# Kernel tuning notes

Hardware: AMD Instinct MI355X
Metric: run time of the kernel (lower is better)

## Reference

```python
import jax, jax.numpy as jnp
import numpy as np

D_MODEL = 1024
N_HEADS = 16
D_HEAD = D_MODEL // N_HEADS
B, T = 4, 2048


def setup_inputs() -> dict:
    key = jax.random.key(0)
    k1, k2, k3 = jax.random.split(key, 3)
    x = jax.random.normal(k1, (B, T, D_MODEL), dtype=jnp.float32)
    # nn.Linear(d_model, 3*d_model, bias=False): y = x @ W_qkv (stored here as [d, 3d])
    W_qkv = jax.random.normal(k2, (D_MODEL, 3 * D_MODEL), dtype=jnp.float32) * (D_MODEL ** -0.5)
    W_out = jax.random.normal(k3, (D_MODEL, D_MODEL), dtype=jnp.float32) * (D_MODEL ** -0.5)
    # causal mask: 1 = keep, 0 = masked (masked_fill(mask == 0, -inf))
    mask = jnp.tril(jnp.ones((T, T), dtype=jnp.int32))
    return {"x": x, "W_qkv": W_qkv, "W_out": W_out, "mask": mask}


def reference(x, W_qkv, W_out, mask):
    Bb, Tt, C = x.shape
    qkv = (x @ W_qkv).reshape(Bb, Tt, 3, N_HEADS, D_HEAD)
    q, k, v = qkv[:, :, 0], qkv[:, :, 1], qkv[:, :, 2]  # each [B,T,H,Dh]
    # scores: [B,H,T,T]
    attn = jnp.einsum('bthd,bshd->bhts', q, k) / jnp.sqrt(jnp.float32(D_HEAD))
    attn = jnp.where(mask == 0, -jnp.inf, attn)
    attn = jax.nn.softmax(attn, axis=-1)
    out = jnp.einsum('bhts,bshd->bthd', attn, v).reshape(Bb, Tt, C)
    return out @ W_out
```

## Files before the change

kernel.cpp:

```cpp
#include <hip/hip_runtime.h>
#include <cstdint>
#include <cstddef>


#define D_MODEL 1024
#define NHEADS  16
#define DHEAD   64
#define BATCH   4
#define SEQ     2048

typedef __attribute__((ext_vector_type(8))) _Float16 half8;
typedef __attribute__((ext_vector_type(4))) _Float16 half4;
typedef __attribute__((ext_vector_type(4))) float    f32x4;

__device__ __forceinline__ void async_copy16(const _Float16* g, _Float16* l) {
    __builtin_amdgcn_global_load_lds(
        (const __attribute__((address_space(1))) uint32_t*)g,
        (__attribute__((address_space(3))) uint32_t*)l, 16, 0, 0);
}

__device__ __forceinline__ float fast_exp2(float x) {
#if __has_builtin(__builtin_amdgcn_exp2f)
    return __builtin_amdgcn_exp2f(x);
#else
    return exp2f(x);
#endif
}

__global__ void cast_f32_f16(const float* __restrict__ in,
                             _Float16* __restrict__ out) {
    int i = blockIdx.x * blockDim.x + threadIdx.x;
    float4 v = *(const float4*)(in + (size_t)i * 4);
    half4 o;
    o.x = (_Float16)v.x; o.y = (_Float16)v.y;
    o.z = (_Float16)v.z; o.w = (_Float16)v.w;
    *(half4*)(out + (size_t)i * 4) = o;
}

__global__ void transpose_cast(const float* __restrict__ in,
                               _Float16* __restrict__ out, int R, int C) {
    __shared__ float tile[32][33];
    int c0 = blockIdx.x * 32, r0 = blockIdx.y * 32;
    int tx = threadIdx.x, ty = threadIdx.y;
    #pragma unroll
    for (int i = 0; i < 32; i += 8)
        tile[ty + i][tx] = in[(size_t)(r0 + ty + i) * C + c0 + tx];
    __syncthreads();
    #pragma unroll
    for (int i = 0; i < 32; i += 8)
        out[(size_t)(c0 + ty + i) * R + r0 + tx] = (_Float16)tile[tx][ty + i];
}

__global__ void gemm_qkv(const _Float16* __restrict__ A,
                         const _Float16* __restrict__ Bt,
                         _Float16* __restrict__ QK,
                         _Float16* __restrict__ Vtg) {
    __shared__ __attribute__((aligned(16))) _Float16 smem[128 * 132];
    _Float16* As = smem;
    _Float16* Bs = smem + 8192;

    const int tid  = threadIdx.x;
    const int w    = tid >> 6, lane = tid & 63;
    const int l15  = lane & 15, quad = lane >> 4;
    const int wm   = w >> 1, wn = w & 1;
    const int row0 = blockIdx.y * 128, col0 = blockIdx.x * 128;
    const int K = 1024;

    f32x4 acc[4][4];
    #pragma unroll
    for (int i = 0; i < 4; i++)
        #pragma unroll
        for (int j = 0; j < 4; j++)
            acc[i][j] = (f32x4){0.f, 0.f, 0.f, 0.f};

    const int lr  = lane >> 3;
    const int src = (lane & 7) ^ lr;

    for (int k0 = 0; k0 < K; k0 += 64) {
        __syncthreads();
        #pragma unroll
        for (int q = 0; q < 4; q++) {
            async_copy16(A  + (size_t)(row0 + q * 32 + w * 8 + lr) * K + k0 + src * 8,
                         &As[(q * 32 + w * 8) * 64]);
            async_copy16(Bt + (size_t)(col0 + q * 32 + w * 8 + lr) * K + k0 + src * 8,
                         &Bs[(q * 32 + w * 8) * 64]);
        }
        __syncthreads();

        half8 af[2][4], bfm[2][4];
        #pragma unroll
        for (int i = 0; i < 4; i++) {
            const int ar = wm * 64 + i * 16 + l15;
            const int rs = ar & 7;
            #pragma unroll
            for (int kk = 0; kk < 2; kk++)
                af[kk][i] = *(const half8*)&As[ar * 64 + ((kk * 4 + quad) ^ rs) * 8];
        }
        #pragma unroll
        for (int j = 0; j < 4; j++) {
            const int br = wn * 64 + j * 16 + l15;
            const int rs = br & 7;
            #pragma unroll
            for (int kk = 0; kk < 2; kk++)
                bfm[kk][j] = *(const half8*)&Bs[br * 64 + ((kk * 4 + quad) ^ rs) * 8];
        }
        #pragma unroll
        for (int kk = 0; kk < 2; kk++)
            #pragma unroll
            for (int i = 0; i < 4; i++)
                #pragma unroll
                for (int j = 0; j < 4; j++)
                    acc[i][j] = __builtin_amdgcn_mfma_f32_16x16x32_f16(
                        af[kk][i], bfm[kk][j], acc[i][j], 0, 0, 0);
    }

    if (blockIdx.x < 16) {
        #pragma unroll
        for (int i = 0; i < 4; i++) {
            int row = row0 + wm * 64 + i * 16 + quad * 4;
            #pragma unroll
            for (int j = 0; j < 4; j++) {
                int col = col0 + wn * 64 + j * 16 + l15;
                #pragma unroll
                for (int r = 0; r < 4; r++)
                    QK[(size_t)(row + r) * 2048 + col] = (_Float16)acc[i][j][r];
            }
        }
    } else {
        __syncthreads();
        #pragma unroll
        for (int i = 0; i < 4; i++) {
            int tl = wm * 64 + i * 16 + quad * 4;
            #pragma unroll
            for (int j = 0; j < 4; j++) {
                int vl = wn * 64 + j * 16 + l15;
                half4 pk;
                #pragma unroll
                for (int r = 0; r < 4; r++) pk[r] = (_Float16)acc[i][j][r];
                *(half4*)&smem[vl * 132 + tl] = pk;
            }
        }
        __syncthreads();
        const int bb = row0 >> 11, tb = row0 & 2047;
        const int rr0 = tid >> 4;
        const int cc  = (tid & 15) * 8;
        #pragma unroll
        for (int s = 0; s < 8; s++) {
            int vl = rr0 + s * 16;
            int vcol = (col0 - 2048) + vl;
            int hh = vcol >> 6, d = vcol & 63;
            *(half8*)&Vtg[((size_t)((bb * 16 + hh) * 64 + d)) * 2048 + tb + cc] =
                *(const half8*)&smem[vl * 132 + cc];
        }
    }
}

__global__ void gemm_out(const _Float16* __restrict__ A,
                         const _Float16* __restrict__ Bt,
                         float* __restrict__ Cf, int N, int K) {
    __shared__ __attribute__((aligned(16))) _Float16 As[128 * 32];
    __shared__ __attribute__((aligned(16))) _Float16 Bs[128 * 32];

    const int tid  = threadIdx.x;
    const int w    = tid >> 6, lane = tid & 63;
    const int l15  = lane & 15, quad = lane >> 4;
    const int wm   = w >> 1, wn = w & 1;
    const int row0 = blockIdx.y * 128, col0 = blockIdx.x * 128;

    f32x4 acc[4][4];
    #pragma unroll
    for (int i = 0; i < 4; i++)
        #pragma unroll
        for (int j = 0; j < 4; j++)
            acc[i][j] = (f32x4){0.f, 0.f, 0.f, 0.f};

    const int r0i = tid >> 2, c0i = tid & 3;
    const int r1i = (256 + tid) >> 2;

    for (int k0 = 0; k0 < K; k0 += 32) {
        __syncthreads();
        async_copy16(A  + (size_t)(row0 + r0i) * K + k0 + c0i * 8, &As[(w * 64) * 8]);
        async_copy16(A  + (size_t)(row0 + r1i) * K + k0 + c0i * 8, &As[(256 + w * 64) * 8]);
        async_copy16(Bt + (size_t)(col0 + r0i) * K + k0 + c0i * 8, &Bs[(w * 64) * 8]);
        async_copy16(Bt + (size_t)(col0 + r1i) * K + k0 + c0i * 8, &Bs[(256 + w * 64) * 8]);
        __syncthreads();

        half8 af[4], bfm[4];
        #pragma unroll
        for (int i = 0; i < 4; i++)
            af[i] = *(const half8*)&As[(wm * 64 + i * 16 + l15) * 32 + quad * 8];
        #pragma unroll
        for (int j = 0; j < 4; j++)
            bfm[j] = *(const half8*)&Bs[(wn * 64 + j * 16 + l15) * 32 + quad * 8];
        #pragma unroll
        for (int i = 0; i < 4; i++)
            #pragma unroll
            for (int j = 0; j < 4; j++)
                acc[i][j] = __builtin_amdgcn_mfma_f32_16x16x32_f16(
                    af[i], bfm[j], acc[i][j], 0, 0, 0);
    }

    #pragma unroll
    for (int i = 0; i < 4; i++) {
        int row = row0 + wm * 64 + i * 16 + quad * 4;
        #pragma unroll
        for (int j = 0; j < 4; j++) {
            int col = col0 + wn * 64 + j * 16 + l15;
            #pragma unroll
            for (int r = 0; r < 4; r++)
                Cf[(size_t)(row + r) * N + col] = acc[i][j][r];
        }
    }
}

#define PREFETCH(t)                                                          \
    do {                                                                     \
        const _Float16* kp_ = kb + (size_t)((t) * 128 + srow) * 2048 + sc;   \
        kr0 = *(const half8*)kp_;                                            \
        kr1 = *(const half8*)(kp_ + (size_t)32 * 2048);                      \
        kr2 = *(const half8*)(kp_ + (size_t)64 * 2048);                      \
        kr3 = *(const half8*)(kp_ + (size_t)96 * 2048);                      \
        const _Float16* vp_ = vb + (size_t)srow * 2048 + (t) * 128 + sc;     \
        vr0 = *(const half8*)vp_;                                            \
        vr1 = *(const half8*)(vp_ + 64);                                     \
        vr2 = *(const half8*)(vp_ + (size_t)32 * 2048);                      \
        vr3 = *(const half8*)(vp_ + (size_t)32 * 2048 + 64);                 \
    } while (0)

__global__ __launch_bounds__(256, 2) void flash_attn(
        const _Float16* __restrict__ qk, const _Float16* __restrict__ vt,
        _Float16* __restrict__ obuf) {
    const int h = blockIdx.x, pr = blockIdx.y, b = blockIdx.z;
    const int tid = threadIdx.x;
    const int w = tid >> 6, lane = tid & 63;
    const int l15 = lane & 15, quad = lane >> 4;

    __shared__ __attribute__((aligned(16))) _Float16 Ks[128 * 72];
    __shared__ __attribute__((aligned(16))) _Float16 Vs[64 * 136];
    __shared__ __attribute__((aligned(16))) _Float16 Pl[4][32 * 136];

    const _Float16* kb = qk + (size_t)b * SEQ * 2048 + D_MODEL + h * 64;
    const _Float16* vb = vt + (size_t)(b * 16 + h) * 64 * 2048;

    const int srow = tid >> 3;
    const int sc   = (tid & 7) * 8;

    const _Float16 QSCL = (_Float16)0.18033688f;

    #pragma unroll 1
    for (int phase = 0; phase < 2; ++phase) {
        const int tq = phase ? (15 - pr) : pr;
        const int q0 = tq * 128;
        const int n_iter = tq + 1;

        half8 qf[2][2];
        #pragma unroll
        for (int g = 0; g < 2; g++) {
            const _Float16* qp = qk
                + ((size_t)(b * SEQ + q0 + w * 32 + g * 16 + l15)) * 2048
                + h * DHEAD + quad * 8;
            qf[g][0] = *(const half8*)qp;
            qf[g][1] = *(const half8*)(qp + 32);
            #pragma unroll
            for (int j = 0; j < 8; j++) {
                qf[g][0][j] *= QSCL;
                qf[g][1][j] *= QSCL;
            }
        }

        f32x4 o[2][4];
        float l_acc[2] = {0.f, 0.f};
        #pragma unroll
        for (int g = 0; g < 2; g++)
            #pragma unroll
            for (int d = 0; d < 4; d++) o[g][d] = (f32x4){0.f, 0.f, 0.f, 0.f};

        half8 kr0, kr1, kr2, kr3, vr0, vr1, vr2, vr3;
        PREFETCH(0);

        #pragma unroll 1
        for (int it = 0; it < n_iter; ++it) {
            __syncthreads();
            *(half8*)&Ks[(srow      ) * 72 + sc] = kr0;
            *(half8*)&Ks[(srow + 32 ) * 72 + sc] = kr1;
            *(half8*)&Ks[(srow + 64 ) * 72 + sc] = kr2;
            *(half8*)&Ks[(srow + 96 ) * 72 + sc] = kr3;
            *(half8*)&Vs[srow * 136 + sc]             = vr0;
            *(half8*)&Vs[srow * 136 + sc + 64]        = vr1;
            *(half8*)&Vs[(srow + 32) * 136 + sc]      = vr2;
            *(half8*)&Vs[(srow + 32) * 136 + sc + 64] = vr3;
            __syncthreads();

            if (it + 1 < n_iter) PREFETCH(it + 1);

            #pragma unroll
            for (int hh = 0; hh < 2; hh++) {
                f32x4 st[2][4];
                __builtin_amdgcn_s_setprio(1);
                #pragma unroll
                for (int n4 = 0; n4 < 4; n4++) {
                    const int nt = hh * 4 + n4;
                    half8 ka0 = *(const half8*)&Ks[(nt * 16 + l15) * 72 + quad * 8];
                    half8 ka1 = *(const half8*)&Ks[(nt * 16 + l15) * 72 + 32 + quad * 8];
                    #pragma unroll
                    for (int g = 0; g < 2; g++) {
                        f32x4 acc = (f32x4){0.f, 0.f, 0.f, 0.f};
                        acc = __builtin_amdgcn_mfma_f32_16x16x32_f16(ka0, qf[g][0], acc, 0, 0, 0);
                        acc = __builtin_amdgcn_mfma_f32_16x16x32_f16(ka1, qf[g][1], acc, 0, 0, 0);
                        st[g][n4] = acc;
                    }
                }
                __builtin_amdgcn_s_setprio(0);

                #pragma unroll
                for (int g = 0; g < 2; g++) {
                    const int c0 = __builtin_amdgcn_readfirstlane(
                        q0 + w * 32 + g * 16 - 128 * it);
                    if (c0 < 127) {
                        #pragma unroll
                        for (int n4 = 0; n4 < 4; n4++)
                            #pragma unroll
                            for (int r = 0; r < 4; r++)
                                if ((hh * 4 + n4) * 16 + quad * 4 + r - l15 > c0)
                                    st[g][n4][r] = -INFINITY;
                    }
                    #pragma unroll
                    for (int n4 = 0; n4 < 4; n4++) {
                        const int nt = hh * 4 + n4;
                        float p0 = fast_exp2(st[g][n4][0]);
                        float p1 = fast_exp2(st[g][n4][1]);
                        float p2 = fast_exp2(st[g][n4][2]);
                        float p3 = fast_exp2(st[g][n4][3]);
                        l_acc[g] += (p0 + p1) + (p2 + p3);
                        auto lo = __builtin_amdgcn_cvt_pkrtz(p0, p1);
                        auto hi = __builtin_amdgcn_cvt_pkrtz(p2, p3);
                        half4 pk;
                        pk[0] = (_Float16)lo[0]; pk[1] = (_Float16)lo[1];
                        pk[2] = (_Float16)hi[0]; pk[3] = (_Float16)hi[1];
                        *(half4*)&Pl[w][(g * 16 + l15) * 136 + nt * 16 + quad * 4] = pk;
                    }
                }
            }
            asm volatile("s_waitcnt lgkmcnt(0)" ::: "memory");

            __builtin_amdgcn_s_setprio(1);
            #pragma unroll
            for (int kf = 0; kf < 4; kf++) {
                half8 pf0 = *(const half8*)&Pl[w][l15 * 136 + kf * 32 + quad * 8];
                half8 pf1 = *(const half8*)&Pl[w][(16 + l15) * 136 + kf * 32 + quad * 8];
                #pragma unroll
                for (int dt = 0; dt < 4; dt++) {
                    half8 vf = *(const half8*)&Vs[(dt * 16 + l15) * 136 + kf * 32 + quad * 8];
                    o[0][dt] = __builtin_amdgcn_mfma_f32_16x16x32_f16(pf0, vf, o[0][dt], 0, 0, 0);
                    o[1][dt] = __builtin_amdgcn_mfma_f32_16x16x32_f16(pf1, vf, o[1][dt], 0, 0, 0);
                }
            }
            __builtin_amdgcn_s_setprio(0);
        }

        #pragma unroll
        for (int g = 0; g < 2; g++) {
            float l = l_acc[g];
            l += __shfl_xor(l, 16);
            l += __shfl_xor(l, 32);
            float linv[4];
            #pragma unroll
            for (int r = 0; r < 4; r++)
                linv[r] = 1.0f / __shfl(l, quad * 4 + r, 16);

            _Float16* ob = obuf
                + ((size_t)(b * SEQ + q0 + w * 32 + g * 16 + quad * 4)) * D_MODEL
                + h * DHEAD;
            #pragma unroll
            for (int r = 0; r < 4; r++) {
                #pragma unroll
                for (int dt = 0; dt < 4; dt++)
                    ob[(size_t)r * D_MODEL + dt * 16 + l15] =
                        (_Float16)(o[g][dt][r] * linv[r]);
            }
        }
        __syncthreads();
    }
}

extern "C" void kernel_launch(void* const* d_in, const int* in_sizes, int n_in,
                              void* d_out, int out_size, void* d_ws, size_t ws_size,
                              hipStream_t stream) {
    const float* x    = (const float*)d_in[0];
    const float* Wqkv = (const float*)d_in[1];
    const float* Wout = (const float*)d_in[2];
    float* out = (float*)d_out;

    char* ws = (char*)d_ws;
    _Float16* Xh   = (_Float16*)(ws);
    _Float16* WqT  = (_Float16*)(ws + ((size_t)16 << 20));
    _Float16* WoT  = (_Float16*)(ws + ((size_t)23 << 20));
    _Float16* QKb  = (_Float16*)(ws + ((size_t)26 << 20));
    _Float16* Vtg  = (_Float16*)(ws + ((size_t)58 << 20));
    _Float16* Obuf = (_Float16*)(ws + ((size_t)74 << 20));

    cast_f32_f16<<<8192, 256, 0, stream>>>(x, Xh);
    transpose_cast<<<dim3(96, 32), dim3(32, 8), 0, stream>>>(Wqkv, WqT, 1024, 3072);
    transpose_cast<<<dim3(32, 32), dim3(32, 8), 0, stream>>>(Wout, WoT, 1024, 1024);
    gemm_qkv<<<dim3(24, 64), 256, 0, stream>>>(Xh, WqT, QKb, Vtg);
    flash_attn<<<dim3(NHEADS, 8, BATCH), 256, 0, stream>>>(QKb, Vtg, Obuf);
    gemm_out<<<dim3(8, 64), 256, 0, stream>>>(Obuf, WoT, out, 1024, 1024);
}
```

Baseline: 258.5 us.

## Fuse input prep kernels and widen gemm_out K-tile with swizzled LDS

Merges the x cast and both weight transpose-casts into a single prep launch indexed by block id, removing two kernel launches and their gaps. gemm_out now loads 64-wide K tiles per iteration with an XOR-swizzled LDS layout, halving the number of barrier pairs and aiming to avoid LDS bank conflicts on fragment reads. This costs more shared memory per block, which may reduce occupancy. The early return in the cast branch sits before a __syncthreads, but that is safe because the branch is uniform across each block.

```diff
diff --git a/kernel.cpp b/kernel.cpp
--- a/kernel.cpp
+++ b/kernel.cpp
@@ -27,21 +27,32 @@
 #endif
 }
 
-__global__ void cast_f32_f16(const float* __restrict__ in,
-                             _Float16* __restrict__ out) {
-    int i = blockIdx.x * blockDim.x + threadIdx.x;
-    float4 v = *(const float4*)(in + (size_t)i * 4);
-    half4 o;
-    o.x = (_Float16)v.x; o.y = (_Float16)v.y;
-    o.z = (_Float16)v.z; o.w = (_Float16)v.w;
-    *(half4*)(out + (size_t)i * 4) = o;
-}
-
-__global__ void transpose_cast(const float* __restrict__ in,
-                               _Float16* __restrict__ out, int R, int C) {
+__global__ void prep(const float* __restrict__ x,  _Float16* __restrict__ Xh,
+                     const float* __restrict__ Wq, _Float16* __restrict__ WqT,
+                     const float* __restrict__ Wo, _Float16* __restrict__ WoT) {
     __shared__ float tile[32][33];
-    int c0 = blockIdx.x * 32, r0 = blockIdx.y * 32;
-    int tx = threadIdx.x, ty = threadIdx.y;
+    const int blk = blockIdx.x, tid = threadIdx.x;
+
+    if (blk < 8192) {
+        const size_t i = (size_t)blk * 256 + tid;
+        float4 v = *(const float4*)(x + i * 4);
+        half4 o;
+        o.x = (_Float16)v.x; o.y = (_Float16)v.y;
+        o.z = (_Float16)v.z; o.w = (_Float16)v.w;
+        *(half4*)(Xh + i * 4) = o;
+        return;
+    }
+
+    const float* in; _Float16* out; int R, C, bx, by;
+    if (blk < 8192 + 3072) {
+        const int b = blk - 8192;
+        in = Wq; out = WqT; R = 1024; C = 3072; bx = b % 96; by = b / 96;
+    } else {
+        const int b = blk - 8192 - 3072;
+        in = Wo; out = WoT; R = 1024; C = 1024; bx = b % 32; by = b / 32;
+    }
+    const int tx = tid & 31, ty = tid >> 5;
+    const int c0 = bx * 32, r0 = by * 32;
     #pragma unroll
     for (int i = 0; i < 32; i += 8)
         tile[ty + i][tx] = in[(size_t)(r0 + ty + i) * C + c0 + tx];
@@ -158,8 +169,9 @@
 __global__ void gemm_out(const _Float16* __restrict__ A,
                          const _Float16* __restrict__ Bt,
                          float* __restrict__ Cf, int N, int K) {
-    __shared__ __attribute__((aligned(16))) _Float16 As[128 * 32];
-    __shared__ __attribute__((aligned(16))) _Float16 Bs[128 * 32];
+    __shared__ __attribute__((aligned(16))) _Float16 smem[128 * 128];
+    _Float16* As = smem;
+    _Float16* Bs = smem + 8192;
 
     const int tid  = threadIdx.x;
     const int w    = tid >> 6, lane = tid & 63;
@@ -174,30 +186,45 @@
         for (int j = 0; j < 4; j++)
             acc[i][j] = (f32x4){0.f, 0.f, 0.f, 0.f};
 
-    const int r0i = tid >> 2, c0i = tid & 3;
-    const int r1i = (256 + tid) >> 2;
-
-    for (int k0 = 0; k0 < K; k0 += 32) {
-        __syncthreads();
-        async_copy16(A  + (size_t)(row0 + r0i) * K + k0 + c0i * 8, &As[(w * 64) * 8]);
-        async_copy16(A  + (size_t)(row0 + r1i) * K + k0 + c0i * 8, &As[(256 + w * 64) * 8]);
-        async_copy16(Bt + (size_t)(col0 + r0i) * K + k0 + c0i * 8, &Bs[(w * 64) * 8]);
-        async_copy16(Bt + (size_t)(col0 + r1i) * K + k0 + c0i * 8, &Bs[(256 + w * 64) * 8]);
-        __syncthreads();
-
-        half8 af[4], bfm[4];
-        #pragma unroll
-        for (int i = 0; i < 4; i++)
-            af[i] = *(const half8*)&As[(wm * 64 + i * 16 + l15) * 32 + quad * 8];
-        #pragma unroll
-        for (int j = 0; j < 4; j++)
-            bfm[j] = *(const half8*)&Bs[(wn * 64 + j * 16 + l15) * 32 + quad * 8];
-        #pragma unroll
-        for (int i = 0; i < 4; i++)
-            #pragma unroll
-            for (int j = 0; j < 4; j++)
-                acc[i][j] = __builtin_amdgcn_mfma_f32_16x16x32_f16(
-                    af[i], bfm[j], acc[i][j], 0, 0, 0);
+    const int lr  = lane >> 3;
+    const int src = (lane & 7) ^ lr;
+
+    for (int k0 = 0; k0 < K; k0 += 64) {
+        __syncthreads();
+        #pragma unroll
+        for (int q = 0; q < 4; q++) {
+            async_copy16(A  + (size_t)(row0 + q * 32 + w * 8 + lr) * K + k0 + src * 8,
+                         &As[(q * 32 + w * 8) * 64]);
+            async_copy16(Bt + (size_t)(col0 + q * 32 + w * 8 + lr) * K + k0 + src * 8,
+                         &Bs[(q * 32 + w * 8) * 64]);
+        }
+        __syncthreads();
+
+        half8 af[2][4], bfm[2][4];
+        #pragma unroll
+        for (int i = 0; i < 4; i++) {
+            const int ar = wm * 64 + i * 16 + l15;
+            const int rs = ar & 7;
+            #pragma unroll
+            for (int kk = 0; kk < 2; kk++)
+                af[kk][i] = *(const half8*)&As[ar * 64 + ((kk * 4 + quad) ^ rs) * 8];
+        }
+        #pragma unroll
+        for (int j = 0; j < 4; j++) {
+            const int br = wn * 64 + j * 16 + l15;
+            const int rs = br & 7;
+            #pragma unroll
+            for (int kk = 0; kk < 2; kk++)
+                bfm[kk][j] = *(const half8*)&Bs[br * 64 + ((kk * 4 + quad) ^ rs) * 8];
+        }
+        #pragma unroll
+        for (int kk = 0; kk < 2; kk++)
+            #pragma unroll
+            for (int i = 0; i < 4; i++)
+                #pragma unroll
+                for (int j = 0; j < 4; j++)
+                    acc[i][j] = __builtin_amdgcn_mfma_f32_16x16x32_f16(
+                        af[kk][i], bfm[kk][j], acc[i][j], 0, 0, 0);
     }
 
     #pragma unroll
@@ -399,9 +426,7 @@
     _Float16* Vtg  = (_Float16*)(ws + ((size_t)58 << 20));
     _Float16* Obuf = (_Float16*)(ws + ((size_t)74 << 20));
 
-    cast_f32_f16<<<8192, 256, 0, stream>>>(x, Xh);
-    transpose_cast<<<dim3(96, 32), dim3(32, 8), 0, stream>>>(Wqkv, WqT, 1024, 3072);
-    transpose_cast<<<dim3(32, 32), dim3(32, 8), 0, stream>>>(Wout, WoT, 1024, 1024);
+    prep<<<8192 + 3072 + 1024, 256, 0, stream>>>(x, Xh, Wqkv, WqT, Wout, WoT);
     gemm_qkv<<<dim3(24, 64), 256, 0, stream>>>(Xh, WqT, QKb, Vtg);
     flash_attn<<<dim3(NHEADS, 8, BATCH), 256, 0, stream>>>(QKb, Vtg, Obuf);
     gemm_out<<<dim3(8, 64), 256, 0, stream>>>(Obuf, WoT, out, 1024, 1024);
```

Result: faster. 247.3 us (-4.3%).
